# Kernel optimization log

Hardware: AMD Instinct MI355X
Metric: run time of the kernel (lower is better)

Reference implementation:

```python
import jax, jax.numpy as jnp
import numpy as np

K = 16          # buckets per codeblock (2**treeDepth)
DEPTH = 4       # tree depth
C = 256         # codeblockCount
IN_FEATURES = 4096
OUT_FEATURES = 4096
N_ROWS = 4096

_BASE_TREE = np.array([
    [-1,-1,0,-1,0,0,0,-1,0,0,0,0,0,0,0],[-1,-1,0,-1,0,0,0,1,0,0,0,0,0,0,0],
    [-1,-1,0,1,0,0,0,0,-1,0,0,0,0,0,0],[-1,-1,0,1,0,0,0,0,1,0,0,0,0,0,0],
    [-1,1,0,0,-1,0,0,0,0,-1,0,0,0,0,0],[-1,1,0,0,-1,0,0,0,0,1,0,0,0,0,0],
    [-1,1,0,0,1,0,0,0,0,0,-1,0,0,0,0],[-1,1,0,0,1,0,0,0,0,0,1,0,0,0,0],
    [1,0,-1,0,0,-1,0,0,0,0,0,-1,0,0,0],[1,0,-1,0,0,-1,0,0,0,0,0,1,0,0,0],
    [1,0,-1,0,0,1,0,0,0,0,0,0,-1,0,0],[1,0,-1,0,0,1,0,0,0,0,0,0,1,0,0],
    [1,0,1,0,0,0,-1,0,0,0,0,0,0,-1,0],[1,0,1,0,0,0,-1,0,0,0,0,0,0,1,0],
    [1,0,1,0,0,0,1,0,0,0,0,0,0,0,-1],[1,0,1,0,0,0,1,0,0,0,0,0,0,0,1]],
    dtype=np.float32)

def _make_tree_des_matrix(c):
    # NOTE: original code initializes with ONES, then overwrites diagonal blocks
    m = np.ones((c * K, c * (K - 1)), dtype=np.float32)
    for i in range(c):
        m[i*K:(i+1)*K, i*(K-1):(i+1)*(K-1)] = _BASE_TREE
    return m

def _make_selection_matrix(c):
    base = np.zeros((K - 1, DEPTH), dtype=np.float32)
    base[0, 0] = 1.0
    for i in range(1, K - 1):
        base[i, int(np.log2(i + 1))] = 1.0
    m = np.zeros((c * (K - 1), c * DEPTH), dtype=np.float32)
    for i in range(c):
        m[i*(K-1):(i+1)*(K-1), i*DEPTH:(i+1)*DEPTH] = base
    return m

def setup_inputs() -> dict:
    key = jax.random.key(0)
    k1, k2, k3, k4 = jax.random.split(key, 4)
    inputMatrix = jax.random.normal(k1, (N_ROWS, IN_FEATURES), dtype=jnp.float32)
    dims = jax.random.randint(k2, (C * DEPTH,), 0, IN_FEATURES)
    selection_matrix = jnp.asarray(_make_selection_matrix(C))
    thresholds = jax.random.normal(k3, (C * (K - 1), 1), dtype=jnp.float32)
    tree_des_mat = jnp.asarray(_make_tree_des_matrix(C))
    lut = jax.random.normal(k4, (OUT_FEATURES, C, K), dtype=jnp.float32)
    return {"inputMatrix": inputMatrix, "dims": dims,
            "selection_matrix": selection_matrix, "thresholds": thresholds,
            "tree_des_mat": tree_des_mat, "lut": lut}

def reference(inputMatrix, dims, selection_matrix, thresholds, tree_des_mat, lut):
    n = inputMatrix.shape[0]
    c = lut.shape[1]
    # gather the tree-split feature dims: (N, C*DEPTH)
    chosen = inputMatrix[:, dims]
    # (C*15, N)
    subtracted = selection_matrix @ chosen.T - thresholds
    tanh_h = jnp.tanh(subtracted)
    sign_ste = jnp.sign(subtracted) - jax.lax.stop_gradient(tanh_h) + tanh_h
    # (C*16, N) -> (N, C, 16)
    tree_result = (tree_des_mat @ sign_ste).T.reshape(n, c, K)
    encoding_soft = jax.nn.softmax(tree_result, axis=2)
    index = jnp.argmax(encoding_soft, axis=2)
    encoding_hard = jax.nn.one_hot(index, K, dtype=encoding_soft.dtype)
    Encoded = encoding_hard - jax.lax.stop_gradient(encoding_soft) + encoding_soft
    # LUT lookup: einsum 'nij,kij->nki' + sum over i, fused to 'nij,kij->nk'
    out = jnp.einsum('nij,kij->nk', Encoded, lut)
    return out
```

## Files before the change

### kernel.cpp

```cpp
#include <hip/hip_runtime.h>

#define N_ROWS 4096
#define IN_F   4096
#define OUT_F  4096
#define C_CB   256
#define KDIM   4096

typedef short bf16x8 __attribute__((ext_vector_type(8)));
typedef float f32x4  __attribute__((ext_vector_type(4)));

union ABFrag { unsigned long long u[2]; bf16x8 v; };

__device__ __forceinline__ unsigned int f2bf(float f) {
    unsigned int u = __builtin_bit_cast(unsigned int, f);
    return (u + 0x7FFFu + ((u >> 16) & 1u)) >> 16;
}

__global__ __launch_bounds__(256) void k_idx(const float* __restrict__ input,
                                             const int* __restrict__ dims,
                                             const float* __restrict__ thr,
                                             unsigned char* __restrict__ idx4) {
    __shared__ float rowS[IN_F];
    __shared__ float thrS[C_CB * 15];
    __shared__ int   dimS[C_CB * 4];
    const int n = blockIdx.x;
    const int t = threadIdx.x;

    #pragma unroll
    for (int i = 0; i < 4; i++) dimS[i * 256 + t] = dims[i * 256 + t];
    #pragma unroll
    for (int i = 0; i < 15; i++) thrS[i * 256 + t] = thr[i * 256 + t];
    const float* row = input + (size_t)n * IN_F;
    #pragma unroll
    for (int i = 0; i < 4; i++) {
        float4 v = *(const float4*)(row + i * 1024 + t * 4);
        *(float4*)(rowS + i * 1024 + t * 4) = v;
    }
    __syncthreads();

    const int c = t;
    int4 d = *(const int4*)(dimS + c * 4);
    const float* th = thrS + c * 15;
    float x0 = rowS[d.x], x1 = rowS[d.y], x2 = rowS[d.z], x3 = rowS[d.w];
    int b0 = x0 > th[0];
    int j1 = 1 + b0;
    int b1 = x1 > th[j1];
    int j2 = 2 * j1 + 1 + b1;
    int b2 = x2 > th[j2];
    int j3 = 2 * j2 + 1 + b2;
    int b3 = x3 > th[j3];
    int idx = (b0 << 3) | (b1 << 2) | (b2 << 1) | b3;
    int other = __shfl_xor(idx, 1);
    if (!(c & 1))
        idx4[(c >> 1) * N_ROWS + n] = (unsigned char)(idx | (other << 4));
}

__global__ void k_cvt(const float* __restrict__ lut, unsigned short* __restrict__ lutb) {
    const int i = (blockIdx.x * blockDim.x + threadIdx.x) * 8;
    float4 a = *(const float4*)(lut + i);
    float4 b = *(const float4*)(lut + i + 4);
    uint4 o;
    o.x = f2bf(a.x) | (f2bf(a.y) << 16);
    o.y = f2bf(a.z) | (f2bf(a.w) << 16);
    o.z = f2bf(b.x) | (f2bf(b.y) << 16);
    o.w = f2bf(b.z) | (f2bf(b.w) << 16);
    *(uint4*)(lutb + i) = o;
}

#define BM 128
#define BN 256
#define BKT 64
#define BSTAGE (BN * BKT * 2)
#define NT (KDIM / BKT)

template<bool STAGE_FP32>
__global__ __launch_bounds__(256, 2) void k_gemm(const unsigned short* __restrict__ lutb,
                                                 const float* __restrict__ lutf,
                                                 const unsigned char* __restrict__ idx4,
                                                 float* __restrict__ out) {
    __shared__ unsigned char smem[8192 + 2 * BSTAGE];
    unsigned char* ish  = smem;
    unsigned char* bsh0 = smem + 8192;
    unsigned char* bsh1 = smem + 8192 + BSTAGE;

    const int t   = threadIdx.x;
    const int l15 = t & 15;
    const int q   = (t >> 4) & 3;
    const int w   = t >> 6;
    const int wm  = w >> 1, wn = w & 1;

    const int bid = blockIdx.x;
    const int bx  = ((bid & 7) << 1) | ((bid >> 3) & 1);
    const int by  = bid >> 4;
    const int m0  = by * BM;
    const int n0  = bx * BN;

    auto stageIdx = [&](int h) {
        #pragma unroll
        for (int qq = 0; qq < 2; qq++) {
            int L = qq * 256 + t;
            const unsigned char* g = idx4 + (size_t)(h * 64 + (L >> 3)) * N_ROWS + m0 + (L & 7) * 16;
            __builtin_amdgcn_global_load_lds(
                (const __attribute__((address_space(1))) void*)g,
                (__attribute__((address_space(3))) void*)(ish + L * 16), 16, 0, 0);
        }
    };

    auto stageB = [&](unsigned char* dst, int kbn) {
        #pragma unroll
        for (int qq = 0; qq < 8; qq++) {
            int L = qq * 256 + t;
            int r = L >> 3, p = L & 7;
            int c = p ^ (r & 7);
            const unsigned short* g = lutb + (size_t)(n0 + r) * KDIM + kbn + c * 8;
            __builtin_amdgcn_global_load_lds(
                (const __attribute__((address_space(1))) void*)g,
                (__attribute__((address_space(3))) void*)(dst + L * 16), 16, 0, 0);
        }
    };
    auto stageB32 = [&](unsigned char* dst, int kbn) {
        #pragma unroll
        for (int qq = 0; qq < 8; qq++) {
            int L = qq * 256 + t;
            int r = L >> 3, p = L & 7;
            int c = p ^ (r & 7);
            const float* g = lutf + (size_t)(n0 + r) * KDIM + kbn + c * 8;
            float4 f0 = *(const float4*)g;
            float4 f1 = *(const float4*)(g + 4);
            uint4 o;
            o.x = f2bf(f0.x) | (f2bf(f0.y) << 16);
            o.y = f2bf(f0.z) | (f2bf(f0.w) << 16);
            o.z = f2bf(f1.x) | (f2bf(f1.y) << 16);
            o.w = f2bf(f1.z) | (f2bf(f1.w) << 16);
            *(uint4*)(dst + L * 16) = o;
        }
    };

    f32x4 acc[4][8];
    #pragma unroll
    for (int mi = 0; mi < 4; mi++)
        #pragma unroll
        for (int ni = 0; ni < 8; ni++)
            acc[mi][ni] = (f32x4){0.f, 0.f, 0.f, 0.f};

    const int xorv = l15 & 7;
    const int bRowByte = (wn * 128 + l15) * (BKT * 2);
    const int aByte = wm * 64 + l15 * 4;
    const int qh4  = (q >> 1) * 4;
    const unsigned int sub8 = (q & 1) << 3;

    auto readPhase = [&](const unsigned char* src, int s, int kb, ABFrag (&bf)[8], unsigned int& w32) {
        const int chunkOff = ((s * 4 + q) ^ xorv) * 16;
        #pragma unroll
        for (int ni = 0; ni < 8; ni++)
            bf[ni].v = *(const bf16x8*)(src + bRowByte + ni * (16 * BKT * 2) + chunkOff);
        w32 = *(const unsigned int*)(ish + ((((kb >> 5) + s) & 63) * 128) + aByte);
    };
    auto mfmaPhase = [&](const ABFrag (&bf)[8], unsigned int w32) {
        ABFrag af[4];
        #pragma unroll
        for (int mi = 0; mi < 4; mi++) {
            unsigned int T = (w32 >> (mi * 8 + qh4)) & 0xFu;
            unsigned int rel = T - sub8;
            unsigned long long sh = 0x3F80ull << ((rel & 3) << 4);
            af[mi].u[0] = (rel < 4u) ? sh : 0ull;
            af[mi].u[1] = ((rel - 4u) < 4u) ? sh : 0ull;
        }
        #pragma unroll
        for (int mi = 0; mi < 4; mi++)
            #pragma unroll
            for (int ni = 0; ni < 8; ni++)
                acc[mi][ni] = __builtin_amdgcn_mfma_f32_16x16x32_bf16(
                    af[mi].v, bf[ni].v, acc[mi][ni], 0, 0, 0);
    };

    if (!STAGE_FP32) {
        stageIdx(0);
        stageB(bsh0, 0);
        stageB(bsh1, BKT);
        asm volatile("s_waitcnt vmcnt(8)" ::: "memory");
        __builtin_amdgcn_s_barrier();
        __builtin_amdgcn_sched_barrier(0);

        unsigned char* cur = bsh0;
        unsigned char* nxt = bsh1;
        ABFrag bf0[8], bf1[8];
        unsigned int w0, w1;
        for (int tt = 0; tt < NT; tt++) {
            const int kb = tt * BKT;
            readPhase(cur, 0, kb, bf0, w0);
            asm volatile("s_waitcnt lgkmcnt(0)" ::: "memory");
            __builtin_amdgcn_sched_barrier(0);
            readPhase(cur, 1, kb, bf1, w1);
            __builtin_amdgcn_sched_barrier(0);
            __builtin_amdgcn_s_setprio(1);
            mfmaPhase(bf0, w0);
            __builtin_amdgcn_s_setprio(0);
            asm volatile("s_waitcnt lgkmcnt(0)" ::: "memory");
            __builtin_amdgcn_sched_barrier(0);
            __builtin_amdgcn_s_barrier();
            __builtin_amdgcn_sched_barrier(0);
            if (tt == 31) stageIdx(1);
            if (tt + 2 < NT) stageB(cur, kb + 2 * BKT);
            __builtin_amdgcn_sched_barrier(0);
            __builtin_amdgcn_s_setprio(1);
            mfmaPhase(bf1, w1);
            __builtin_amdgcn_s_setprio(0);
            if (tt + 2 < NT) asm volatile("s_waitcnt vmcnt(8)" ::: "memory");
            else             asm volatile("s_waitcnt vmcnt(0)" ::: "memory");
            __builtin_amdgcn_s_barrier();
            __builtin_amdgcn_sched_barrier(0);
            unsigned char* tmp = cur; cur = nxt; nxt = tmp;
        }
    } else {
        stageIdx(0);
        asm volatile("s_waitcnt vmcnt(0)" ::: "memory");
        __syncthreads();
        ABFrag bfx[8];
        unsigned int wx;
        for (int tt = 0; tt < NT; tt++) {
            const int kb = tt * BKT;
            if (tt == 32) stageIdx(1);
            stageB32(bsh0, kb);
            __syncthreads();
            #pragma unroll
            for (int s = 0; s < 2; s++) {
                readPhase(bsh0, s, kb, bfx, wx);
                mfmaPhase(bfx, wx);
            }
            __syncthreads();
        }
    }

    #pragma unroll
    for (int mi = 0; mi < 4; mi++) {
        #pragma unroll
        for (int ni = 0; ni < 8; ni++) {
            const int col = n0 + wn * 128 + ni * 16 + l15;
            #pragma unroll
            for (int r = 0; r < 4; r++) {
                const int row = m0 + wm * 64 + 4 * (q * 4 + r) + mi;
                out[(size_t)row * OUT_F + col] = acc[mi][ni][r];
            }
        }
    }
}

extern "C" void kernel_launch(void* const* d_in, const int* in_sizes, int n_in,
                              void* d_out, int out_size, void* d_ws, size_t ws_size,
                              hipStream_t stream) {
    const float* input = (const float*)d_in[0];
    const int*   dims  = (const int*)d_in[1];
    const float* thr   = (const float*)d_in[3];
    const float* lut   = (const float*)d_in[5];
    float* out = (float*)d_out;

    const size_t lutbBytes = (size_t)OUT_F * KDIM * 2;
    const size_t idxBytes  = (size_t)(C_CB / 2) * N_ROWS;

    const int nblocks = (OUT_F / BN) * (N_ROWS / BM);

    if (ws_size >= lutbBytes + idxBytes) {
        unsigned short* lutb = (unsigned short*)d_ws;
        unsigned char*  idx4 = (unsigned char*)d_ws + lutbBytes;
        k_idx<<<N_ROWS, C_CB, 0, stream>>>(input, dims, thr, idx4);
        k_cvt<<<(OUT_F * KDIM) / (256 * 8), 256, 0, stream>>>(lut, lutb);
        k_gemm<false><<<nblocks, 256, 0, stream>>>(lutb, lut, idx4, out);
    } else {
        unsigned char* idx4 = (unsigned char*)d_ws;
        k_idx<<<N_ROWS, C_CB, 0, stream>>>(input, dims, thr, idx4);
        k_gemm<true><<<nblocks, 256, 0, stream>>>(nullptr, lut, idx4, out);
    }
}
```

Measured before the change: 284.7 us.

## Switch GEMM to 32x32x16 MFMA and merge index and LUT-convert kernels

Replaces the 16x16x32 bf16 MFMA tiling with 32x32x16 MFMA tiles. This changes the fragment reads from LDS, the one-hot A-fragment construction from the packed indices, and the output write mapping. It also fuses the index computation and the LUT fp32-to-bf16 conversion into one launch, split by block ID. The goals are fewer LDS fragment reads per FLOP, higher MFMA efficiency, and one less kernel launch. The risk is that the new lane/row mapping and the LDS bank access pattern could be wrong or conflict more.

```diff
diff --git a/kernel.cpp b/kernel.cpp
--- a/kernel.cpp
+++ b/kernel.cpp
@@ -8,6 +8,7 @@
 
 typedef short bf16x8 __attribute__((ext_vector_type(8)));
 typedef float f32x4  __attribute__((ext_vector_type(4)));
+typedef float f32x16 __attribute__((ext_vector_type(16)));
 
 union ABFrag { unsigned long long u[2]; bf16x8 v; };
 
@@ -16,55 +17,60 @@
     return (u + 0x7FFFu + ((u >> 16) & 1u)) >> 16;
 }
 
-__global__ __launch_bounds__(256) void k_idx(const float* __restrict__ input,
-                                             const int* __restrict__ dims,
-                                             const float* __restrict__ thr,
-                                             unsigned char* __restrict__ idx4) {
+#define CVT_BLOCKS ((OUT_F * KDIM) / (256 * 8))
+
+__global__ __launch_bounds__(256) void k_prep(const float* __restrict__ input,
+                                              const int* __restrict__ dims,
+                                              const float* __restrict__ thr,
+                                              unsigned char* __restrict__ idx4,
+                                              const float* __restrict__ lut,
+                                              unsigned short* __restrict__ lutb) {
     __shared__ float rowS[IN_F];
     __shared__ float thrS[C_CB * 15];
     __shared__ int   dimS[C_CB * 4];
-    const int n = blockIdx.x;
+    const int b = blockIdx.x;
     const int t = threadIdx.x;
 
-    #pragma unroll
-    for (int i = 0; i < 4; i++) dimS[i * 256 + t] = dims[i * 256 + t];
-    #pragma unroll
-    for (int i = 0; i < 15; i++) thrS[i * 256 + t] = thr[i * 256 + t];
-    const float* row = input + (size_t)n * IN_F;
-    #pragma unroll
-    for (int i = 0; i < 4; i++) {
-        float4 v = *(const float4*)(row + i * 1024 + t * 4);
-        *(float4*)(rowS + i * 1024 + t * 4) = v;
-    }
-    __syncthreads();
-
-    const int c = t;
-    int4 d = *(const int4*)(dimS + c * 4);
-    const float* th = thrS + c * 15;
-    float x0 = rowS[d.x], x1 = rowS[d.y], x2 = rowS[d.z], x3 = rowS[d.w];
-    int b0 = x0 > th[0];
-    int j1 = 1 + b0;
-    int b1 = x1 > th[j1];
-    int j2 = 2 * j1 + 1 + b1;
-    int b2 = x2 > th[j2];
-    int j3 = 2 * j2 + 1 + b2;
-    int b3 = x3 > th[j3];
-    int idx = (b0 << 3) | (b1 << 2) | (b2 << 1) | b3;
-    int other = __shfl_xor(idx, 1);
-    if (!(c & 1))
-        idx4[(c >> 1) * N_ROWS + n] = (unsigned char)(idx | (other << 4));
-}
-
-__global__ void k_cvt(const float* __restrict__ lut, unsigned short* __restrict__ lutb) {
-    const int i = (blockIdx.x * blockDim.x + threadIdx.x) * 8;
-    float4 a = *(const float4*)(lut + i);
-    float4 b = *(const float4*)(lut + i + 4);
-    uint4 o;
-    o.x = f2bf(a.x) | (f2bf(a.y) << 16);
-    o.y = f2bf(a.z) | (f2bf(a.w) << 16);
-    o.z = f2bf(b.x) | (f2bf(b.y) << 16);
-    o.w = f2bf(b.z) | (f2bf(b.w) << 16);
-    *(uint4*)(lutb + i) = o;
+    if (b < N_ROWS) {
+        const int n = b;
+        #pragma unroll
+        for (int i = 0; i < 4; i++) dimS[i * 256 + t] = dims[i * 256 + t];
+        #pragma unroll
+        for (int i = 0; i < 15; i++) thrS[i * 256 + t] = thr[i * 256 + t];
+        const float* row = input + (size_t)n * IN_F;
+        #pragma unroll
+        for (int i = 0; i < 4; i++) {
+            float4 v = *(const float4*)(row + i * 1024 + t * 4);
+            *(float4*)(rowS + i * 1024 + t * 4) = v;
+        }
+        __syncthreads();
+
+        const int c = t;
+        int4 d = *(const int4*)(dimS + c * 4);
+        const float* th = thrS + c * 15;
+        float x0 = rowS[d.x], x1 = rowS[d.y], x2 = rowS[d.z], x3 = rowS[d.w];
+        int b0 = x0 > th[0];
+        int j1 = 1 + b0;
+        int b1 = x1 > th[j1];
+        int j2 = 2 * j1 + 1 + b1;
+        int b2 = x2 > th[j2];
+        int j3 = 2 * j2 + 1 + b2;
+        int b3 = x3 > th[j3];
+        int idx = (b0 << 3) | (b1 << 2) | (b2 << 1) | b3;
+        int other = __shfl_xor(idx, 1);
+        if (!(c & 1))
+            idx4[(c >> 1) * N_ROWS + n] = (unsigned char)(idx | (other << 4));
+    } else {
+        const int i = ((b - N_ROWS) * 256 + t) * 8;
+        float4 a = *(const float4*)(lut + i);
+        float4 f = *(const float4*)(lut + i + 4);
+        uint4 o;
+        o.x = f2bf(a.x) | (f2bf(a.y) << 16);
+        o.y = f2bf(a.z) | (f2bf(a.w) << 16);
+        o.z = f2bf(f.x) | (f2bf(f.y) << 16);
+        o.w = f2bf(f.z) | (f2bf(f.w) << 16);
+        *(uint4*)(lutb + i) = o;
+    }
 }
 
 #define BM 128
@@ -84,8 +90,8 @@
     unsigned char* bsh1 = smem + 8192 + BSTAGE;
 
     const int t   = threadIdx.x;
-    const int l15 = t & 15;
-    const int q   = (t >> 4) & 3;
+    const int r31 = t & 31;
+    const int h   = (t >> 5) & 1;
     const int w   = t >> 6;
     const int wm  = w >> 1, wn = w & 1;
 
@@ -95,11 +101,11 @@
     const int m0  = by * BM;
     const int n0  = bx * BN;
 
-    auto stageIdx = [&](int h) {
+    auto stageIdx = [&](int hh) {
         #pragma unroll
         for (int qq = 0; qq < 2; qq++) {
             int L = qq * 256 + t;
-            const unsigned char* g = idx4 + (size_t)(h * 64 + (L >> 3)) * N_ROWS + m0 + (L & 7) * 16;
+            const unsigned char* g = idx4 + (size_t)(hh * 64 + (L >> 3)) * N_ROWS + m0 + (L & 7) * 16;
             __builtin_amdgcn_global_load_lds(
                 (const __attribute__((address_space(1))) void*)g,
                 (__attribute__((address_space(3))) void*)(ish + L * 16), 16, 0, 0);
@@ -136,42 +142,49 @@
         }
     };
 
-    f32x4 acc[4][8];
+    f32x16 acc[2][4];
     #pragma unroll
-    for (int mi = 0; mi < 4; mi++)
-        #pragma unroll
-        for (int ni = 0; ni < 8; ni++)
-            acc[mi][ni] = (f32x4){0.f, 0.f, 0.f, 0.f};
-
-    const int xorv = l15 & 7;
-    const int bRowByte = (wn * 128 + l15) * (BKT * 2);
-    const int aByte = wm * 64 + l15 * 4;
-    const int qh4  = (q >> 1) * 4;
-    const unsigned int sub8 = (q & 1) << 3;
-
-    auto readPhase = [&](const unsigned char* src, int s, int kb, ABFrag (&bf)[8], unsigned int& w32) {
-        const int chunkOff = ((s * 4 + q) ^ xorv) * 16;
-        #pragma unroll
-        for (int ni = 0; ni < 8; ni++)
-            bf[ni].v = *(const bf16x8*)(src + bRowByte + ni * (16 * BKT * 2) + chunkOff);
-        w32 = *(const unsigned int*)(ish + ((((kb >> 5) + s) & 63) * 128) + aByte);
-    };
-    auto mfmaPhase = [&](const ABFrag (&bf)[8], unsigned int w32) {
-        ABFrag af[4];
-        #pragma unroll
-        for (int mi = 0; mi < 4; mi++) {
-            unsigned int T = (w32 >> (mi * 8 + qh4)) & 0xFu;
-            unsigned int rel = T - sub8;
-            unsigned long long sh = 0x3F80ull << ((rel & 3) << 4);
-            af[mi].u[0] = (rel < 4u) ? sh : 0ull;
-            af[mi].u[1] = ((rel - 4u) < 4u) ? sh : 0ull;
-        }
-        #pragma unroll
-        for (int mi = 0; mi < 4; mi++)
-            #pragma unroll
-            for (int ni = 0; ni < 8; ni++)
-                acc[mi][ni] = __builtin_amdgcn_mfma_f32_16x16x32_bf16(
-                    af[mi].v, bf[ni].v, acc[mi][ni], 0, 0, 0);
+    for (int ms = 0; ms < 2; ms++)
+        #pragma unroll
+        for (int ns = 0; ns < 4; ns++)
+            acc[ms][ns] = (f32x16){0.f,0.f,0.f,0.f,0.f,0.f,0.f,0.f,
+                                   0.f,0.f,0.f,0.f,0.f,0.f,0.f,0.f};
+
+    const int xorv = r31 & 7;
+    const int bBase = (wn * 128 + r31) * (BKT * 2);
+    const int aByte = wm * 64 + 2 * r31;
+    const unsigned int sub8 = h << 3;
+
+    auto readPhase = [&](const unsigned char* src, int s, int kb,
+                         ABFrag (&bf)[2][4], unsigned int& w16) {
+        #pragma unroll
+        for (int cb = 0; cb < 2; cb++) {
+            const int chunkOff = ((s * 4 + cb * 2 + h) ^ xorv) * 16;
+            #pragma unroll
+            for (int ns = 0; ns < 4; ns++)
+                bf[cb][ns].v = *(const bf16x8*)(src + bBase + ns * (32 * BKT * 2) + chunkOff);
+        }
+        w16 = *(const unsigned short*)(ish + ((((kb >> 5) + s) & 63) * 128) + aByte);
+    };
+    auto mfmaPhase = [&](const ABFrag (&bf)[2][4], unsigned int w16) {
+        #pragma unroll
+        for (int cb = 0; cb < 2; cb++) {
+            ABFrag af[2];
+            #pragma unroll
+            for (int ms = 0; ms < 2; ms++) {
+                unsigned int T = (w16 >> (ms * 8 + cb * 4)) & 0xFu;
+                unsigned int rel = T - sub8;
+                unsigned long long sh = 0x3F80ull << ((rel & 3) << 4);
+                af[ms].u[0] = (rel < 4u) ? sh : 0ull;
+                af[ms].u[1] = ((rel - 4u) < 4u) ? sh : 0ull;
+            }
+            #pragma unroll
+            for (int ms = 0; ms < 2; ms++)
+                #pragma unroll
+                for (int ns = 0; ns < 4; ns++)
+                    acc[ms][ns] = __builtin_amdgcn_mfma_f32_32x32x16_bf16(
+                        af[ms].v, bf[cb][ns].v, acc[ms][ns], 0, 0, 0);
+        }
     };
 
     if (!STAGE_FP32) {
@@ -184,7 +197,7 @@
 
         unsigned char* cur = bsh0;
         unsigned char* nxt = bsh1;
-        ABFrag bf0[8], bf1[8];
+        ABFrag bf0[2][4], bf1[2][4];
         unsigned int w0, w1;
         for (int tt = 0; tt < NT; tt++) {
             const int kb = tt * BKT;
@@ -216,7 +229,7 @@
         stageIdx(0);
         asm volatile("s_waitcnt vmcnt(0)" ::: "memory");
         __syncthreads();
-        ABFrag bfx[8];
+        ABFrag bfx[2][4];
         unsigned int wx;
         for (int tt = 0; tt < NT; tt++) {
             const int kb = tt * BKT;
@@ -233,14 +246,15 @@
     }
 
     #pragma unroll
-    for (int mi = 0; mi < 4; mi++) {
-        #pragma unroll
-        for (int ni = 0; ni < 8; ni++) {
-            const int col = n0 + wn * 128 + ni * 16 + l15;
-            #pragma unroll
-            for (int r = 0; r < 4; r++) {
-                const int row = m0 + wm * 64 + 4 * (q * 4 + r) + mi;
-                out[(size_t)row * OUT_F + col] = acc[mi][ni][r];
+    for (int ms = 0; ms < 2; ms++) {
+        #pragma unroll
+        for (int ns = 0; ns < 4; ns++) {
+            const int col = n0 + wn * 128 + ns * 32 + r31;
+            #pragma unroll
+            for (int reg = 0; reg < 16; reg++) {
+                const int mr  = (reg & 3) + 8 * (reg >> 2) + 4 * h;
+                const int row = m0 + wm * 64 + 2 * mr + ms;
+                out[(size_t)row * OUT_F + col] = acc[ms][ns][reg];
             }
         }
     }
@@ -263,12 +277,11 @@
     if (ws_size >= lutbBytes + idxBytes) {
         unsigned short* lutb = (unsigned short*)d_ws;
         unsigned char*  idx4 = (unsigned char*)d_ws + lutbBytes;
-        k_idx<<<N_ROWS, C_CB, 0, stream>>>(input, dims, thr, idx4);
-        k_cvt<<<(OUT_F * KDIM) / (256 * 8), 256, 0, stream>>>(lut, lutb);
+        k_prep<<<N_ROWS + CVT_BLOCKS, 256, 0, stream>>>(input, dims, thr, idx4, lut, lutb);
         k_gemm<false><<<nblocks, 256, 0, stream>>>(lutb, lut, idx4, out);
     } else {
         unsigned char* idx4 = (unsigned char*)d_ws;
-        k_idx<<<N_ROWS, C_CB, 0, stream>>>(input, dims, thr, idx4);
+        k_prep<<<N_ROWS, 256, 0, stream>>>(input, dims, thr, idx4, lut, nullptr);
         k_gemm<true><<<nblocks, 256, 0, stream>>>(nullptr, lut, idx4, out);
     }
 }
```

Measured after the change: 299.1 us. 5.0% more time.

## Merge prep kernels and restructure GEMM main loop to prefetch B fragments

Applied to the files above, without the earlier changes.

The index-building and LUT bf16-conversion kernels are merged into one launch, with block ranges choosing the role, which removes one kernel launch and lets both jobs run at the same time. The GEMM now stages all index bytes into a doubled 16 KB LDS region up front instead of reloading the second half midway. The main loop is reorganised to read the next tile's first B fragment from LDS before the second MFMA phase and to use one barrier per iteration instead of two. In exchange it waits with vmcnt(0) every iteration, which may expose global-load latency, and the larger LDS footprint could reduce occupancy.

```diff
diff --git a/kernel.cpp b/kernel.cpp
--- a/kernel.cpp
+++ b/kernel.cpp
@@ -16,55 +16,60 @@
     return (u + 0x7FFFu + ((u >> 16) & 1u)) >> 16;
 }
 
-__global__ __launch_bounds__(256) void k_idx(const float* __restrict__ input,
-                                             const int* __restrict__ dims,
-                                             const float* __restrict__ thr,
-                                             unsigned char* __restrict__ idx4) {
+#define CVT_BLOCKS ((OUT_F * KDIM) / (256 * 8))
+
+__global__ __launch_bounds__(256) void k_prep(const float* __restrict__ input,
+                                              const int* __restrict__ dims,
+                                              const float* __restrict__ thr,
+                                              unsigned char* __restrict__ idx4,
+                                              const float* __restrict__ lut,
+                                              unsigned short* __restrict__ lutb) {
     __shared__ float rowS[IN_F];
     __shared__ float thrS[C_CB * 15];
     __shared__ int   dimS[C_CB * 4];
-    const int n = blockIdx.x;
+    const int b = blockIdx.x;
     const int t = threadIdx.x;
 
-    #pragma unroll
-    for (int i = 0; i < 4; i++) dimS[i * 256 + t] = dims[i * 256 + t];
-    #pragma unroll
-    for (int i = 0; i < 15; i++) thrS[i * 256 + t] = thr[i * 256 + t];
-    const float* row = input + (size_t)n * IN_F;
-    #pragma unroll
-    for (int i = 0; i < 4; i++) {
-        float4 v = *(const float4*)(row + i * 1024 + t * 4);
-        *(float4*)(rowS + i * 1024 + t * 4) = v;
-    }
-    __syncthreads();
-
-    const int c = t;
-    int4 d = *(const int4*)(dimS + c * 4);
-    const float* th = thrS + c * 15;
-    float x0 = rowS[d.x], x1 = rowS[d.y], x2 = rowS[d.z], x3 = rowS[d.w];
-    int b0 = x0 > th[0];
-    int j1 = 1 + b0;
-    int b1 = x1 > th[j1];
-    int j2 = 2 * j1 + 1 + b1;
-    int b2 = x2 > th[j2];
-    int j3 = 2 * j2 + 1 + b2;
-    int b3 = x3 > th[j3];
-    int idx = (b0 << 3) | (b1 << 2) | (b2 << 1) | b3;
-    int other = __shfl_xor(idx, 1);
-    if (!(c & 1))
-        idx4[(c >> 1) * N_ROWS + n] = (unsigned char)(idx | (other << 4));
-}
-
-__global__ void k_cvt(const float* __restrict__ lut, unsigned short* __restrict__ lutb) {
-    const int i = (blockIdx.x * blockDim.x + threadIdx.x) * 8;
-    float4 a = *(const float4*)(lut + i);
-    float4 b = *(const float4*)(lut + i + 4);
-    uint4 o;
-    o.x = f2bf(a.x) | (f2bf(a.y) << 16);
-    o.y = f2bf(a.z) | (f2bf(a.w) << 16);
-    o.z = f2bf(b.x) | (f2bf(b.y) << 16);
-    o.w = f2bf(b.z) | (f2bf(b.w) << 16);
-    *(uint4*)(lutb + i) = o;
+    if (b < N_ROWS) {
+        const int n = b;
+        #pragma unroll
+        for (int i = 0; i < 4; i++) dimS[i * 256 + t] = dims[i * 256 + t];
+        #pragma unroll
+        for (int i = 0; i < 15; i++) thrS[i * 256 + t] = thr[i * 256 + t];
+        const float* row = input + (size_t)n * IN_F;
+        #pragma unroll
+        for (int i = 0; i < 4; i++) {
+            float4 v = *(const float4*)(row + i * 1024 + t * 4);
+            *(float4*)(rowS + i * 1024 + t * 4) = v;
+        }
+        __syncthreads();
+
+        const int c = t;
+        int4 d = *(const int4*)(dimS + c * 4);
+        const float* th = thrS + c * 15;
+        float x0 = rowS[d.x], x1 = rowS[d.y], x2 = rowS[d.z], x3 = rowS[d.w];
+        int b0 = x0 > th[0];
+        int j1 = 1 + b0;
+        int b1 = x1 > th[j1];
+        int j2 = 2 * j1 + 1 + b1;
+        int b2 = x2 > th[j2];
+        int j3 = 2 * j2 + 1 + b2;
+        int b3 = x3 > th[j3];
+        int idx = (b0 << 3) | (b1 << 2) | (b2 << 1) | b3;
+        int other = __shfl_xor(idx, 1);
+        if (!(c & 1))
+            idx4[(c >> 1) * N_ROWS + n] = (unsigned char)(idx | (other << 4));
+    } else {
+        const int i = ((b - N_ROWS) * 256 + t) * 8;
+        float4 a = *(const float4*)(lut + i);
+        float4 f = *(const float4*)(lut + i + 4);
+        uint4 o;
+        o.x = f2bf(a.x) | (f2bf(a.y) << 16);
+        o.y = f2bf(a.z) | (f2bf(a.w) << 16);
+        o.z = f2bf(f.x) | (f2bf(f.y) << 16);
+        o.w = f2bf(f.z) | (f2bf(f.w) << 16);
+        *(uint4*)(lutb + i) = o;
+    }
 }
 
 #define BM 128
@@ -78,10 +83,10 @@
                                                  const float* __restrict__ lutf,
                                                  const unsigned char* __restrict__ idx4,
                                                  float* __restrict__ out) {
-    __shared__ unsigned char smem[8192 + 2 * BSTAGE];
+    __shared__ unsigned char smem[16384 + 2 * BSTAGE];
     unsigned char* ish  = smem;
-    unsigned char* bsh0 = smem + 8192;
-    unsigned char* bsh1 = smem + 8192 + BSTAGE;
+    unsigned char* bsh0 = smem + 16384;
+    unsigned char* bsh1 = smem + 16384 + BSTAGE;
 
     const int t   = threadIdx.x;
     const int l15 = t & 15;
@@ -95,11 +100,11 @@
     const int m0  = by * BM;
     const int n0  = bx * BN;
 
-    auto stageIdx = [&](int h) {
-        #pragma unroll
-        for (int qq = 0; qq < 2; qq++) {
+    auto stageIdx = [&]() {
+        #pragma unroll
+        for (int qq = 0; qq < 4; qq++) {
             int L = qq * 256 + t;
-            const unsigned char* g = idx4 + (size_t)(h * 64 + (L >> 3)) * N_ROWS + m0 + (L & 7) * 16;
+            const unsigned char* g = idx4 + (size_t)(L >> 3) * N_ROWS + m0 + (L & 7) * 16;
             __builtin_amdgcn_global_load_lds(
                 (const __attribute__((address_space(1))) void*)g,
                 (__attribute__((address_space(3))) void*)(ish + L * 16), 16, 0, 0);
@@ -149,12 +154,14 @@
     const int qh4  = (q >> 1) * 4;
     const unsigned int sub8 = (q & 1) << 3;
 
-    auto readPhase = [&](const unsigned char* src, int s, int kb, ABFrag (&bf)[8], unsigned int& w32) {
+    auto bfRead = [&](const unsigned char* src, int s, ABFrag (&bf)[8]) {
         const int chunkOff = ((s * 4 + q) ^ xorv) * 16;
         #pragma unroll
         for (int ni = 0; ni < 8; ni++)
             bf[ni].v = *(const bf16x8*)(src + bRowByte + ni * (16 * BKT * 2) + chunkOff);
-        w32 = *(const unsigned int*)(ish + ((((kb >> 5) + s) & 63) * 128) + aByte);
+    };
+    auto wRead = [&](int kb, int s) {
+        return *(const unsigned int*)(ish + ((kb >> 5) + s) * 128 + aByte);
     };
     auto mfmaPhase = [&](const ABFrag (&bf)[8], unsigned int w32) {
         ABFrag af[4];
@@ -175,58 +182,55 @@
     };
 
     if (!STAGE_FP32) {
-        stageIdx(0);
+        stageIdx();
         stageB(bsh0, 0);
         stageB(bsh1, BKT);
         asm volatile("s_waitcnt vmcnt(8)" ::: "memory");
         __builtin_amdgcn_s_barrier();
         __builtin_amdgcn_sched_barrier(0);
 
-        unsigned char* cur = bsh0;
-        unsigned char* nxt = bsh1;
-        ABFrag bf0[8], bf1[8];
-        unsigned int w0, w1;
+        ABFrag bfA[8], bfB[8];
+        bfRead(bsh0, 0, bfA);
+        __builtin_amdgcn_sched_barrier(0);
+
         for (int tt = 0; tt < NT; tt++) {
             const int kb = tt * BKT;
-            readPhase(cur, 0, kb, bf0, w0);
-            asm volatile("s_waitcnt lgkmcnt(0)" ::: "memory");
-            __builtin_amdgcn_sched_barrier(0);
-            readPhase(cur, 1, kb, bf1, w1);
+            unsigned char* cur = (tt & 1) ? bsh1 : bsh0;
+            unsigned char* nxt = (tt & 1) ? bsh0 : bsh1;
+            unsigned int w0 = wRead(kb, 0);
+            bfRead(cur, 1, bfB);
+            unsigned int w1 = wRead(kb, 1);
             __builtin_amdgcn_sched_barrier(0);
             __builtin_amdgcn_s_setprio(1);
-            mfmaPhase(bf0, w0);
+            mfmaPhase(bfA, w0);
             __builtin_amdgcn_s_setprio(0);
             asm volatile("s_waitcnt lgkmcnt(0)" ::: "memory");
             __builtin_amdgcn_sched_barrier(0);
+            asm volatile("s_waitcnt vmcnt(0)" ::: "memory");
             __builtin_amdgcn_s_barrier();
             __builtin_amdgcn_sched_barrier(0);
-            if (tt == 31) stageIdx(1);
             if (tt + 2 < NT) stageB(cur, kb + 2 * BKT);
             __builtin_amdgcn_sched_barrier(0);
+            if (tt + 1 < NT) bfRead(nxt, 0, bfA);
+            __builtin_amdgcn_sched_barrier(0);
             __builtin_amdgcn_s_setprio(1);
-            mfmaPhase(bf1, w1);
+            mfmaPhase(bfB, w1);
             __builtin_amdgcn_s_setprio(0);
-            if (tt + 2 < NT) asm volatile("s_waitcnt vmcnt(8)" ::: "memory");
-            else             asm volatile("s_waitcnt vmcnt(0)" ::: "memory");
-            __builtin_amdgcn_s_barrier();
-            __builtin_amdgcn_sched_barrier(0);
-            unsigned char* tmp = cur; cur = nxt; nxt = tmp;
+            __builtin_amdgcn_sched_barrier(0);
         }
     } else {
-        stageIdx(0);
+        stageIdx();
         asm volatile("s_waitcnt vmcnt(0)" ::: "memory");
         __syncthreads();
         ABFrag bfx[8];
-        unsigned int wx;
         for (int tt = 0; tt < NT; tt++) {
             const int kb = tt * BKT;
-            if (tt == 32) stageIdx(1);
             stageB32(bsh0, kb);
             __syncthreads();
             #pragma unroll
             for (int s = 0; s < 2; s++) {
-                readPhase(bsh0, s, kb, bfx, wx);
-                mfmaPhase(bfx, wx);
+                bfRead(bsh0, s, bfx);
+                mfmaPhase(bfx, wRead(kb, s));
             }
             __syncthreads();
         }
@@ -263,12 +267,11 @@
     if (ws_size >= lutbBytes + idxBytes) {
         unsigned short* lutb = (unsigned short*)d_ws;
         unsigned char*  idx4 = (unsigned char*)d_ws + lutbBytes;
-        k_idx<<<N_ROWS, C_CB, 0, stream>>>(input, dims, thr, idx4);
-        k_cvt<<<(OUT_F * KDIM) / (256 * 8), 256, 0, stream>>>(lut, lutb);
+        k_prep<<<N_ROWS + CVT_BLOCKS, 256, 0, stream>>>(input, dims, thr, idx4, lut, lutb);
         k_gemm<false><<<nblocks, 256, 0, stream>>>(lutb, lut, idx4, out);
     } else {
         unsigned char* idx4 = (unsigned char*)d_ws;
-        k_idx<<<N_ROWS, C_CB, 0, stream>>>(input, dims, thr, idx4);
+        k_prep<<<N_ROWS, 256, 0, stream>>>(input, dims, thr, idx4, lut, nullptr);
         k_gemm<true><<<nblocks, 256, 0, stream>>>(nullptr, lut, idx4, out);
     }
 }
```

New measurement: 290.6 us. 2.1% more time.
